# Performance work log

Hardware: AMD Instinct MI355X
Metric: run time of the kernel (lower is better)

## Reference

```python
import jax, jax.numpy as jnp
import numpy as np


def _conv1x1(X, W, b):
    # X: [B,C,H,W], W: [Cout,Cin], b: [Cout] -> [B,Cout,H,W]
    return jnp.einsum('oc,bchw->bohw', W, X) + b[None, :, None, None]


def setup_inputs() -> dict:
    key = jax.random.key(0)
    ks = jax.random.split(key, 7)
    B, C, H, W = 8, 512, 32, 32
    scale = 1.0 / np.sqrt(C)
    return {
        'X': jax.random.normal(ks[0], (B, C, H, W), dtype=jnp.float32),
        'W_phi': jax.random.normal(ks[1], (C, C), dtype=jnp.float32) * scale,
        'b_phi': jnp.zeros((C,), dtype=jnp.float32),
        'W_theta': jax.random.normal(ks[2], (C, C), dtype=jnp.float32) * scale,
        'b_theta': jnp.zeros((C,), dtype=jnp.float32),
        'W_beta': jax.random.normal(ks[3], (C, C), dtype=jnp.float32) * scale,
        'b_beta': jnp.zeros((C,), dtype=jnp.float32),
    }


def reference(X, W_phi, b_phi, W_theta, b_theta, W_beta, b_beta):
    B, C, H, W = X.shape
    N = H * W
    phi = _conv1x1(X, W_phi, b_phi).reshape(B, -1, N)      # [B,Co,N]
    theta = _conv1x1(X, W_theta, b_theta).reshape(B, -1, N)  # [B,Co,N]
    beta = _conv1x1(X, W_beta, b_beta).reshape(B, -1, N)    # [B,Co,N]
    # attention over spatial positions: scores [B,N,N], row-softmax
    A = jax.nn.softmax(jnp.einsum('bcn,bcm->bnm', phi, theta), axis=-1)
    Z = jnp.einsum('bcn,bnm->bcm', beta, A)                 # [B,Co,N]
    return Z.reshape(B, -1, H, W) + X
```

## Files before the change

### kernel.cpp

```cpp
#include <hip/hip_runtime.h>

typedef __bf16 bf16_t;
typedef __bf16 bf16x4 __attribute__((ext_vector_type(4)));
typedef __bf16 bf16x8 __attribute__((ext_vector_type(8)));
typedef _Float16 f16_t;
typedef _Float16 f16x4 __attribute__((ext_vector_type(4)));
typedef _Float16 f16x8 __attribute__((ext_vector_type(8)));
typedef float  f32x4  __attribute__((ext_vector_type(4)));

#define BK 64
#define BATCH 8
#define CDIM 512
#define NSP 1024
#define SOFF 90.0f


__device__ __forceinline__ void gl2lds16(const void* g, void* l) {
    __builtin_amdgcn_global_load_lds(
        (const __attribute__((address_space(1))) void*)g,
        (__attribute__((address_space(3))) void*)l, 16, 0, 0);
}

template<typename T, int NW, int ROWS>
__device__ __forceinline__ void stageRx64(const T* __restrict__ src, int ld, T* dst) {
    int lane = threadIdx.x & 63;
    int wave = threadIdx.x >> 6;
    constexpr int SPW = (ROWS / 8) / NW;
    int colsw = ((lane & 7) ^ (lane >> 3)) << 3;
#pragma unroll
    for (int c = 0; c < SPW; ++c) {
        int seg = wave * SPW + c;
        int row = (seg << 3) + (lane >> 3);
        gl2lds16(src + (size_t)row * ld + colsw, dst + (seg << 9));
    }
}

__device__ __forceinline__ f32x4 mfma_op(f16x8 a, f16x8 b, f32x4 c) {
    return __builtin_amdgcn_mfma_f32_16x16x32_f16(a, b, c, 0, 0, 0);
}
__device__ __forceinline__ f32x4 mfma_op(bf16x8 a, bf16x8 b, f32x4 c) {
    return __builtin_amdgcn_mfma_f32_16x16x32_bf16(a, b, c, 0, 0, 0);
}

template<typename VT, typename T>
__device__ __forceinline__ void gemm128_4w(const T* __restrict__ A, int lda,
                                           const T* __restrict__ B, int ldb, int K,
                                           T* sA, T* sB, f32x4 acc[4][4]) {
    int lane = threadIdx.x & 63;
    int wave = threadIdx.x >> 6;
    int wr = (wave >> 1) << 6;
    int wc = (wave & 1) << 6;
    int fr = lane & 15;
    int q  = lane >> 4;
    constexpr int HALF = 128 * BK;

    for (int k0 = 0; k0 < K; k0 += 2 * BK) {
        stageRx64<T, 4, 128>(A + k0, lda, sA);
        stageRx64<T, 4, 128>(B + k0, ldb, sB);
        __builtin_amdgcn_sched_barrier(0);
        stageRx64<T, 4, 128>(A + k0 + BK, lda, sA + HALF);
        stageRx64<T, 4, 128>(B + k0 + BK, ldb, sB + HALF);
        __builtin_amdgcn_sched_barrier(0);
        asm volatile("s_waitcnt vmcnt(8)" ::: "memory");
        __builtin_amdgcn_s_barrier();
#pragma unroll
        for (int h = 0; h < 2; ++h) {
            const T* pA = sA + h * HALF;
            const T* pB = sB + h * HALF;
#pragma unroll
            for (int kk = 0; kk < 2; ++kk) {
                int sc = ((((kk << 2) + q) ^ (fr & 7)) << 3);
                VT a[4], b[4];
#pragma unroll
                for (int i = 0; i < 4; ++i)
                    a[i] = *reinterpret_cast<const VT*>(pA + (wr + i*16 + fr)*BK + sc);
#pragma unroll
                for (int j = 0; j < 4; ++j)
                    b[j] = *reinterpret_cast<const VT*>(pB + (wc + j*16 + fr)*BK + sc);
#pragma unroll
                for (int mi = 0; mi < 4; ++mi)
#pragma unroll
                    for (int ni = 0; ni < 4; ++ni)
                        acc[mi][ni] = mfma_op(a[mi], b[ni], acc[mi][ni]);
            }
            if (h == 0) {
                asm volatile("s_waitcnt vmcnt(0)" ::: "memory");
                __builtin_amdgcn_s_barrier();
            }
        }
        __builtin_amdgcn_s_barrier();
    }
}

__device__ __forceinline__ void zero44(f32x4 acc[4][4]) {
#pragma unroll
    for (int i = 0; i < 4; i++)
#pragma unroll
        for (int j = 0; j < 4; j++)
#pragma unroll
            for (int e = 0; e < 4; e++) acc[i][j][e] = 0.0f;
}

__global__ __launch_bounds__(256)
void prep_kernel(const float* __restrict__ X, const float* __restrict__ Wp,
                 const float* __restrict__ Wt, const float* __restrict__ Wb,
                 f16_t* __restrict__ Xt, f16_t* __restrict__ W16) {
    int z = blockIdx.z;
    int tx = threadIdx.x;
    int ty = threadIdx.y;
    if (z == 8) {
        int g = (blockIdx.y * 32 + blockIdx.x) * 256 + ty * 8 + tx;
        if (g < 98304) {
            int i = g << 3;
            int r = i >> 9, c = i & 511;
            const float* src = (r < 512) ? (Wp + ((size_t)r << 9))
                             : (r < 1024) ? (Wt + ((size_t)(r - 512) << 9))
                                          : (Wb + ((size_t)(r - 1024) << 9));
            float4 v0 = *reinterpret_cast<const float4*>(src + c);
            float4 v1 = *reinterpret_cast<const float4*>(src + c + 4);
            f16x8 o;
            o[0]=(f16_t)v0.x; o[1]=(f16_t)v0.y; o[2]=(f16_t)v0.z; o[3]=(f16_t)v0.w;
            o[4]=(f16_t)v1.x; o[5]=(f16_t)v1.y; o[6]=(f16_t)v1.z; o[7]=(f16_t)v1.w;
            *reinterpret_cast<f16x8*>(W16 + i) = o;
        }
        return;
    }
    __shared__ float tile[32][33];
    const float* x = X + (size_t)z * CDIM * NSP;
    int c0 = blockIdx.y * 32, n0 = blockIdx.x * 32;
    float4 v = *reinterpret_cast<const float4*>(x + (size_t)(c0 + ty) * NSP + n0 + tx * 4);
    tile[ty][tx * 4 + 0] = v.x;
    tile[ty][tx * 4 + 1] = v.y;
    tile[ty][tx * 4 + 2] = v.z;
    tile[ty][tx * 4 + 3] = v.w;
    __syncthreads();
    f16x4 o;
#pragma unroll
    for (int i = 0; i < 4; ++i) o[i] = (f16_t)tile[tx * 4 + i][ty];
    *reinterpret_cast<f16x4*>(Xt + (size_t)z * NSP * CDIM + (size_t)(n0 + ty) * CDIM + c0 + tx * 4) = o;
}

__global__ __launch_bounds__(256, 2)
void conv_pt_kernel(const f16_t* __restrict__ Xt, const f16_t* __restrict__ W16,
                    const float* __restrict__ bias_phi, const float* __restrict__ bias_theta,
                    f16_t* __restrict__ phiH, f16_t* __restrict__ thH) {
    __shared__ alignas(16) f16_t sA[2 * 128 * BK], sB[2 * 128 * BK];
    int b = blockIdx.x;
    int j = blockIdx.y;
    int n0 = (j >> 3) << 7;
    int col0 = (j & 7) << 7;
    f32x4 acc[4][4];
    zero44(acc);
    gemm128_4w<f16x8, f16_t>(Xt + ((size_t)b * NSP + n0) * CDIM, CDIM,
                             W16 + (size_t)col0 * CDIM, CDIM, CDIM, sA, sB, acc);

    int lane = threadIdx.x & 63;
    int wave = threadIdx.x >> 6;
    int wr = (wave >> 1) << 6, wc = (wave & 1) << 6;
    int fr = lane & 15, q4 = ((lane >> 4) << 2);

    bool isPhi = (col0 < 512);
    const float* bias = isPhi ? bias_phi : bias_theta;
    f16_t* dh = (isPhi ? phiH : thH) + (size_t)b * NSP * CDIM;
    int oc0 = col0 & 511;
#pragma unroll
    for (int mi = 0; mi < 4; mi++)
#pragma unroll
        for (int ni = 0; ni < 4; ni++) {
            int col = oc0 + wc + ni * 16 + fr;
            float bv = bias[col];
#pragma unroll
            for (int e = 0; e < 4; e++) {
                int row = n0 + wr + mi * 16 + q4 + e;
                dh[(size_t)row * CDIM + col] = (f16_t)(acc[mi][ni][e] + bv);
            }
        }
}

__global__ __launch_bounds__(256, 2)
void sgemm_beta_kernel(const f16_t* __restrict__ Xt, const f16_t* __restrict__ W16,
                       const f16_t* __restrict__ phiH, const f16_t* __restrict__ thH,
                       const float* __restrict__ bias_beta,
                       bf16_t* __restrict__ Et, float* __restrict__ psum,
                       bf16_t* __restrict__ betaB) {
    __shared__ alignas(16) f16_t sA[2 * 128 * BK], sB[2 * 128 * BK];
    int b = blockIdx.x;
    int j = blockIdx.y;
    int lane = threadIdx.x & 63;
    int wave = threadIdx.x >> 6;
    int wr = (wave >> 1) << 6, wc = (wave & 1) << 6;
    int fr = lane & 15, q4 = ((lane >> 4) << 2);
    f32x4 acc[4][4];
    zero44(acc);

    if (j < 64) {
        int n0 = (j >> 3) << 7, m0 = (j & 7) << 7;
        gemm128_4w<f16x8, f16_t>(phiH + ((size_t)b * NSP + n0) * CDIM, CDIM,
                                 thH + ((size_t)b * NSP + m0) * CDIM, CDIM,
                                 CDIM, sA, sB, acc);
        bf16_t* et = Et + (size_t)b * NSP * NSP;
        float p[4][4];
#pragma unroll
        for (int mi = 0; mi < 4; mi++)
#pragma unroll
            for (int e = 0; e < 4; e++) p[mi][e] = 0.0f;
#pragma unroll
        for (int mi = 0; mi < 4; mi++)
#pragma unroll
            for (int ni = 0; ni < 4; ni++) {
                int col = m0 + wc + ni * 16 + fr;
                int rowb = n0 + wr + mi * 16 + q4;
                bf16x4 v;
#pragma unroll
                for (int e = 0; e < 4; e++) {
                    float ev = __expf(acc[mi][ni][e] - SOFF);
                    p[mi][e] += ev;
                    v[e] = (bf16_t)ev;
                }
                *reinterpret_cast<bf16x4*>(et + (size_t)col * NSP + rowb) = v;
            }
#pragma unroll
        for (int mi = 0; mi < 4; mi++)
#pragma unroll
            for (int e = 0; e < 4; e++) {
#pragma unroll
                for (int off = 1; off < 16; off <<= 1)
                    p[mi][e] += __shfl_xor(p[mi][e], off);
            }
        if ((lane & 15) == 0) {
            int pidx = ((j & 7) << 1) + (wc >> 6);
            float* ps = psum + ((size_t)b * 16 + pidx) * NSP;
#pragma unroll
            for (int mi = 0; mi < 4; mi++)
#pragma unroll
                for (int e = 0; e < 4; e++)
                    ps[n0 + wr + mi * 16 + q4 + e] = p[mi][e];
        }
    } else {
        int j2 = j - 64;
        int nb = j2 >> 2, cb = j2 & 3;
        int n0 = nb << 7;
        gemm128_4w<f16x8, f16_t>(Xt + ((size_t)b * NSP + n0) * CDIM, CDIM,
                                 W16 + (size_t)(1024 + cb * 128) * CDIM, CDIM,
                                 CDIM, sA, sB, acc);
        bf16_t* dst = betaB + (size_t)b * CDIM * NSP;
#pragma unroll
        for (int mi = 0; mi < 4; mi++)
#pragma unroll
            for (int ni = 0; ni < 4; ni++) {
                int c = cb * 128 + wc + ni * 16 + fr;
                float bv = bias_beta[c];
                int rowb = n0 + wr + mi * 16 + q4;
                bf16x4 v;
#pragma unroll
                for (int e = 0; e < 4; e++) v[e] = (bf16_t)(acc[mi][ni][e] + bv);
                *reinterpret_cast<bf16x4*>(dst + (size_t)c * NSP + rowb) = v;
            }
    }
}

__global__ __launch_bounds__(512, 4)
void zgemm_kernel(const bf16_t* __restrict__ betaB, const bf16_t* __restrict__ Et,
                  const float* __restrict__ psum, const float* __restrict__ X,
                  float* __restrict__ out) {
    __shared__ float rs[NSP];
    __shared__ alignas(16) bf16_t sA[2 * 64 * BK];
    __shared__ alignas(16) bf16_t sB[2 * 128 * BK];
    int b = blockIdx.x;
    int m0 = blockIdx.y * 128;
    int c0 = blockIdx.z * 64;
    int tid = threadIdx.x;

#pragma unroll
    for (int i = 0; i < 2; ++i) {
        int n = i * 512 + tid;
        float s = 0.f;
#pragma unroll
        for (int pp = 0; pp < 16; ++pp) s += psum[((size_t)b * 16 + pp) * NSP + n];
        rs[n] = 1.0f / s;
    }
    __syncthreads();

    int lane = tid & 63, wave = tid >> 6;
    int fr = lane & 15, q = lane >> 4, q4 = (lane >> 4) << 2;
    int wr = (wave >> 2) << 5;
    int wc = (wave & 3) << 5;
    int ar = lane >> 3, ac = lane & 7;
    int acs = ac ^ ar;

    const bf16_t* A = betaB + ((size_t)b * CDIM + c0) * NSP;
    const bf16_t* B = Et + ((size_t)b * NSP + m0) * NSP;
    f32x4 acc[2][2];
#pragma unroll
    for (int i = 0; i < 2; i++)
#pragma unroll
        for (int jj = 0; jj < 2; jj++)
#pragma unroll
            for (int e = 0; e < 4; e++) acc[i][jj][e] = 0.0f;

    int row = (wave << 3) + ar;

    for (int k0 = 0; k0 < NSP; k0 += 2 * BK) {
        stageRx64<bf16_t, 8, 128>(B + k0, NSP, sB);
        __builtin_amdgcn_sched_barrier(0);
        bf16x8 v0 = *reinterpret_cast<const bf16x8*>(A + (size_t)row * NSP + k0 + ac * 8);
        bf16x8 v1 = *reinterpret_cast<const bf16x8*>(A + (size_t)row * NSP + k0 + BK + ac * 8);
        __builtin_amdgcn_sched_barrier(0);
        stageRx64<bf16_t, 8, 128>(B + k0 + BK, NSP, sB + 128 * BK);
        __builtin_amdgcn_sched_barrier(0);
#pragma unroll
        for (int h = 0; h < 2; ++h) {
            int kh = k0 + h * BK;
            float4 r0v = *reinterpret_cast<const float4*>(&rs[kh + ac * 8]);
            float4 r1v = *reinterpret_cast<const float4*>(&rs[kh + ac * 8 + 4]);
            bf16x8 v = h ? v1 : v0;
            bf16x8 o;
            o[0] = (bf16_t)((float)v[0] * r0v.x);
            o[1] = (bf16_t)((float)v[1] * r0v.y);
            o[2] = (bf16_t)((float)v[2] * r0v.z);
            o[3] = (bf16_t)((float)v[3] * r0v.w);
            o[4] = (bf16_t)((float)v[4] * r1v.x);
            o[5] = (bf16_t)((float)v[5] * r1v.y);
            o[6] = (bf16_t)((float)v[6] * r1v.z);
            o[7] = (bf16_t)((float)v[7] * r1v.w);
            *reinterpret_cast<bf16x8*>(sA + h * 64 * BK + (wave << 9) + ar * 64 + acs * 8) = o;
        }
        asm volatile("s_waitcnt vmcnt(2) lgkmcnt(0)" ::: "memory");
        __builtin_amdgcn_s_barrier();
#pragma unroll
        for (int h = 0; h < 2; ++h) {
            const bf16_t* pA = sA + h * 64 * BK;
            const bf16_t* pB = sB + h * 128 * BK;
#pragma unroll
            for (int kk = 0; kk < 2; ++kk) {
                int sc = ((((kk << 2) + q) ^ (fr & 7)) << 3);
                bf16x8 a[2], bbv[2];
#pragma unroll
                for (int i = 0; i < 2; ++i)
                    a[i] = *reinterpret_cast<const bf16x8*>(pA + (wr + i*16 + fr)*BK + sc);
#pragma unroll
                for (int jj = 0; jj < 2; ++jj)
                    bbv[jj] = *reinterpret_cast<const bf16x8*>(pB + (wc + jj*16 + fr)*BK + sc);
#pragma unroll
                for (int mi = 0; mi < 2; ++mi)
#pragma unroll
                    for (int ni = 0; ni < 2; ++ni)
                        acc[mi][ni] = mfma_op(a[mi], bbv[ni], acc[mi][ni]);
            }
            if (h == 0) {
                asm volatile("s_waitcnt vmcnt(0)" ::: "memory");
                __builtin_amdgcn_s_barrier();
            }
        }
        __builtin_amdgcn_s_barrier();
    }

    const float* xs = X + (size_t)b * CDIM * NSP;
    float* dst = out + (size_t)b * CDIM * NSP;
#pragma unroll
    for (int mi = 0; mi < 2; mi++)
#pragma unroll
        for (int ni = 0; ni < 2; ni++) {
            int col = m0 + wc + ni * 16 + fr;
#pragma unroll
            for (int e = 0; e < 4; e++) {
                int rowo = c0 + wr + mi * 16 + q4 + e;
                size_t idx = (size_t)rowo * NSP + col;
                dst[idx] = acc[mi][ni][e] + xs[idx];
            }
        }
}

extern "C" void kernel_launch(void* const* d_in, const int* in_sizes, int n_in,
                              void* d_out, int out_size, void* d_ws, size_t ws_size,
                              hipStream_t stream) {
    const float* X  = (const float*)d_in[0];
    const float* Wp = (const float*)d_in[1];
    const float* bp = (const float*)d_in[2];
    const float* Wt = (const float*)d_in[3];
    const float* bt = (const float*)d_in[4];
    const float* Wb = (const float*)d_in[5];
    const float* bb = (const float*)d_in[6];
    float* out = (float*)d_out;

    char* ws = (char*)d_ws;
    size_t off = 0;
    auto alloc = [&](size_t bytes) -> char* {
        char* p = ws + off;
        off += (bytes + 255) & ~(size_t)255;
        return p;
    };

    const size_t BNC2 = (size_t)BATCH * NSP * CDIM * 2;
    f16_t*  Xt16  = (f16_t*)alloc(BNC2);
    f16_t*  W16   = (f16_t*)alloc((size_t)1536 * 512 * 2);
    f16_t*  phiH  = (f16_t*)alloc(BNC2);
    f16_t*  thH   = (f16_t*)alloc(BNC2);
    bf16_t* betaB = (bf16_t*)alloc(BNC2);
    bf16_t* Et    = (bf16_t*)alloc((size_t)BATCH * NSP * NSP * 2);
    float*  psum  = (float*)alloc((size_t)BATCH * 16 * NSP * 4);

    prep_kernel<<<dim3(32, 16, 9), dim3(8, 32), 0, stream>>>(X, Wp, Wt, Wb, Xt16, W16);
    conv_pt_kernel<<<dim3(8, 64), dim3(256), 0, stream>>>(Xt16, W16, bp, bt, phiH, thH);
    sgemm_beta_kernel<<<dim3(8, 96), dim3(256), 0, stream>>>(Xt16, W16, phiH, thH,
                                                             bb, Et, psum, betaB);
    zgemm_kernel<<<dim3(8, 8, 8), dim3(512), 0, stream>>>(betaB, Et, psum, X, out);

    (void)in_sizes; (void)n_in; (void)out_size; (void)ws_size;
}
```

Baseline: 66.37 us.

## Replace batch-of-two K loop with rolling two-slot LDS prefetch ring

The 128x128 GEMM helper used by the conv and score kernels now stages each K-slice into a two-slot LDS ring. Before, it loaded two slices, computed both, then drained to a barrier. Now, right after a slot's slice has been consumed and a barrier passed, the load for the slice two steps ahead is issued into that slot, so global loads overlap compute across the whole K loop. The loop is fully unrolled with K known at compile time, which may raise code size and register pressure.

```diff
diff --git a/kernel.cpp b/kernel.cpp
--- a/kernel.cpp
+++ b/kernel.cpp
@@ -42,10 +42,10 @@
     return __builtin_amdgcn_mfma_f32_16x16x32_bf16(a, b, c, 0, 0, 0);
 }
 
-template<typename VT, typename T>
-__device__ __forceinline__ void gemm128_4w(const T* __restrict__ A, int lda,
-                                           const T* __restrict__ B, int ldb, int K,
-                                           T* sA, T* sB, f32x4 acc[4][4]) {
+template<typename VT, typename T, int K>
+__device__ __forceinline__ void gemm128_ring(const T* __restrict__ A, int lda,
+                                             const T* __restrict__ B, int ldb,
+                                             T* sA, T* sB, f32x4 acc[4][4]) {
     int lane = threadIdx.x & 63;
     int wave = threadIdx.x >> 6;
     int wr = (wave >> 1) << 6;
@@ -53,42 +53,44 @@
     int fr = lane & 15;
     int q  = lane >> 4;
     constexpr int HALF = 128 * BK;
-
-    for (int k0 = 0; k0 < K; k0 += 2 * BK) {
-        stageRx64<T, 4, 128>(A + k0, lda, sA);
-        stageRx64<T, 4, 128>(B + k0, ldb, sB);
-        __builtin_amdgcn_sched_barrier(0);
-        stageRx64<T, 4, 128>(A + k0 + BK, lda, sA + HALF);
-        stageRx64<T, 4, 128>(B + k0 + BK, ldb, sB + HALF);
-        __builtin_amdgcn_sched_barrier(0);
-        asm volatile("s_waitcnt vmcnt(8)" ::: "memory");
+    constexpr int NH = K / BK;
+
+    stageRx64<T, 4, 128>(A, lda, sA);
+    stageRx64<T, 4, 128>(B, ldb, sB);
+    __builtin_amdgcn_sched_barrier(0);
+    stageRx64<T, 4, 128>(A + BK, lda, sA + HALF);
+    stageRx64<T, 4, 128>(B + BK, ldb, sB + HALF);
+    __builtin_amdgcn_sched_barrier(0);
+
+#pragma unroll
+    for (int h = 0; h < NH; ++h) {
+        if (h < NH - 1) asm volatile("s_waitcnt vmcnt(8)" ::: "memory");
+        else            asm volatile("s_waitcnt vmcnt(0)" ::: "memory");
         __builtin_amdgcn_s_barrier();
-#pragma unroll
-        for (int h = 0; h < 2; ++h) {
-            const T* pA = sA + h * HALF;
-            const T* pB = sB + h * HALF;
-#pragma unroll
-            for (int kk = 0; kk < 2; ++kk) {
-                int sc = ((((kk << 2) + q) ^ (fr & 7)) << 3);
-                VT a[4], b[4];
-#pragma unroll
-                for (int i = 0; i < 4; ++i)
-                    a[i] = *reinterpret_cast<const VT*>(pA + (wr + i*16 + fr)*BK + sc);
-#pragma unroll
-                for (int j = 0; j < 4; ++j)
-                    b[j] = *reinterpret_cast<const VT*>(pB + (wc + j*16 + fr)*BK + sc);
-#pragma unroll
-                for (int mi = 0; mi < 4; ++mi)
-#pragma unroll
-                    for (int ni = 0; ni < 4; ++ni)
-                        acc[mi][ni] = mfma_op(a[mi], b[ni], acc[mi][ni]);
-            }
-            if (h == 0) {
-                asm volatile("s_waitcnt vmcnt(0)" ::: "memory");
-                __builtin_amdgcn_s_barrier();
-            }
+        const T* pA = sA + (h & 1) * HALF;
+        const T* pB = sB + (h & 1) * HALF;
+#pragma unroll
+        for (int kk = 0; kk < 2; ++kk) {
+            int sc = ((((kk << 2) + q) ^ (fr & 7)) << 3);
+            VT a[4], b[4];
+#pragma unroll
+            for (int i = 0; i < 4; ++i)
+                a[i] = *reinterpret_cast<const VT*>(pA + (wr + i*16 + fr)*BK + sc);
+#pragma unroll
+            for (int j = 0; j < 4; ++j)
+                b[j] = *reinterpret_cast<const VT*>(pB + (wc + j*16 + fr)*BK + sc);
+#pragma unroll
+            for (int mi = 0; mi < 4; ++mi)
+#pragma unroll
+                for (int ni = 0; ni < 4; ++ni)
+                    acc[mi][ni] = mfma_op(a[mi], b[ni], acc[mi][ni]);
         }
         __builtin_amdgcn_s_barrier();
+        if (h + 2 < NH) {
+            stageRx64<T, 4, 128>(A + (h + 2) * BK, lda, sA + (h & 1) * HALF);
+            stageRx64<T, 4, 128>(B + (h + 2) * BK, ldb, sB + (h & 1) * HALF);
+            __builtin_amdgcn_sched_barrier(0);
+        }
     }
 }
 
@@ -151,8 +153,8 @@
     int col0 = (j & 7) << 7;
     f32x4 acc[4][4];
     zero44(acc);
-    gemm128_4w<f16x8, f16_t>(Xt + ((size_t)b * NSP + n0) * CDIM, CDIM,
-                             W16 + (size_t)col0 * CDIM, CDIM, CDIM, sA, sB, acc);
+    gemm128_ring<f16x8, f16_t, CDIM>(Xt + ((size_t)b * NSP + n0) * CDIM, CDIM,
+                                     W16 + (size_t)col0 * CDIM, CDIM, sA, sB, acc);
 
     int lane = threadIdx.x & 63;
     int wave = threadIdx.x >> 6;
@@ -195,9 +197,9 @@
 
     if (j < 64) {
         int n0 = (j >> 3) << 7, m0 = (j & 7) << 7;
-        gemm128_4w<f16x8, f16_t>(phiH + ((size_t)b * NSP + n0) * CDIM, CDIM,
-                                 thH + ((size_t)b * NSP + m0) * CDIM, CDIM,
-                                 CDIM, sA, sB, acc);
+        gemm128_ring<f16x8, f16_t, CDIM>(phiH + ((size_t)b * NSP + n0) * CDIM, CDIM,
+                                         thH + ((size_t)b * NSP + m0) * CDIM, CDIM,
+                                         sA, sB, acc);
         bf16_t* et = Et + (size_t)b * NSP * NSP;
         float p[4][4];
 #pragma unroll
@@ -240,9 +242,9 @@
         int j2 = j - 64;
         int nb = j2 >> 2, cb = j2 & 3;
         int n0 = nb << 7;
-        gemm128_4w<f16x8, f16_t>(Xt + ((size_t)b * NSP + n0) * CDIM, CDIM,
-                                 W16 + (size_t)(1024 + cb * 128) * CDIM, CDIM,
-                                 CDIM, sA, sB, acc);
+        gemm128_ring<f16x8, f16_t, CDIM>(Xt + ((size_t)b * NSP + n0) * CDIM, CDIM,
+                                         W16 + (size_t)(1024 + cb * 128) * CDIM, CDIM,
+                                         sA, sB, acc);
         bf16_t* dst = betaB + (size_t)b * CDIM * NSP;
 #pragma unroll
         for (int mi = 0; mi < 4; mi++)
```

Measured after the change: 64.97 us. -2.1%, faster.
